# Kernel tuning notes

Measured on AMD Instinct MI355X. Metric: run time of the kernel, lower is better.

Reference implementation:

```python
import jax, jax.numpy as jnp
import numpy as np

N = 96        # num_nodes
D = 64        # emb_size / n_hid
BS = 16
T = 13
G = 1         # num_graph

# all N^2 ordered pairs, receiver-major: edge e=i*N+j has receiver i, sender j
_REC = jnp.repeat(jnp.arange(N), N)
_SEND = jnp.tile(jnp.arange(N), N)


def _lin(shape, key, scale=0.05):
    return (jax.random.normal(key, shape, dtype=jnp.float32) * scale)


def setup_inputs() -> dict:
    key = jax.random.key(0)
    ks = jax.random.split(key, 24)
    inp = {
        "skill_seq": jax.random.randint(ks[0], (BS, T), 0, N, dtype=jnp.int32),
        "adj": jax.random.uniform(ks[1], (G, BS, N, N), dtype=jnp.float32),
        "node_embeddings": jax.random.normal(ks[2], (G, N, D), dtype=jnp.float32),
        # edge MLP
        "W_msg1": _lin((2 * D, D), ks[3]), "b_msg1": jnp.zeros((D,), jnp.float32),
        "W_msg2": _lin((D, D), ks[4]),     "b_msg2": jnp.zeros((D,), jnp.float32),
        # GRU hidden projections (no bias)
        "W_hr": _lin((D, D), ks[5]), "W_hi": _lin((D, D), ks[6]), "W_hh": _lin((D, D), ks[7]),
        # GRU input projections (bias)
        "W_ir": _lin((D, D), ks[8]),  "b_ir": jnp.zeros((D,), jnp.float32),
        "W_ii": _lin((D, D), ks[9]),  "b_ii": jnp.zeros((D,), jnp.float32),
        "W_in": _lin((D, D), ks[10]), "b_in": jnp.zeros((D,), jnp.float32),
        # output MLP
        "W_o1": _lin((D, D), ks[11]), "b_o1": jnp.zeros((D,), jnp.float32),
        "W_o2": _lin((D, D), ks[12]), "b_o2": jnp.zeros((D,), jnp.float32),
        "W_o3": _lin((D, D), ks[13]), "b_o3": jnp.zeros((D,), jnp.float32),
    }
    return inp


def _forward(skill_seq, adj, node_embeddings,
             W_msg1, b_msg1, W_msg2, b_msg2,
             W_hr, W_hi, W_hh,
             W_ir, b_ir, W_ii, b_ii, W_in, b_in,
             W_o1, b_o1, W_o2, b_o2, W_o3, b_o3):
    bs, time_steps = skill_seq.shape
    hidden0 = jnp.zeros((G, bs, N, D), dtype=adj.dtype)
    emb = node_embeddings[0]  # [N, D] (num_graph=1)

    def step(hidden, skill_t):
        # gather senders/receivers over the node axis -> [G, bs, N^2, 2D]
        senders = hidden[:, :, _SEND, :]
        receivers = hidden[:, :, _REC, :]
        pre_msg = jnp.concatenate([senders, receivers], axis=-1)
        msg = jnp.tanh(pre_msg @ W_msg1 + b_msg1)        # [G, bs, N^2, D]
        msg = jnp.tanh(msg @ W_msg2 + b_msg2)
        msg = msg.reshape(G, bs, N, N, D)                # receiver i, sender j
        # mask by adjacency and scatter-sum over senders, then /N
        agg = jnp.einsum('gbij,gbijd->gbid', adj, msg) / N   # [G, bs, N, D]
        inputs = emb[skill_t][None, :, None, :]          # [1, bs, 1, D]
        r = jax.nn.sigmoid(inputs @ W_ir + b_ir + agg @ W_hr)
        i = jax.nn.sigmoid(inputs @ W_ii + b_ii + agg @ W_hi)
        n = jnp.tanh(inputs @ W_in + b_in + r * (agg @ W_hh))
        hidden = (1.0 - i) * n + i * hidden
        pred = jax.nn.relu(hidden @ W_o1 + b_o1)
        pred = jax.nn.relu(pred @ W_o2 + b_o2)
        pred = pred @ W_o3 + b_o3                        # [G, bs, N, D]
        return hidden, pred

    skills_t = skill_seq[:, :time_steps - 1].T           # [T-1, bs]
    _, preds = jax.lax.scan(step, hidden0, skills_t)     # [T-1, G, bs, N, D]
    # torch: stack(dim=1) -> [G, T-1, bs, N, D]; transpose(1,2) -> [G, bs, T-1, N, D]
    return jnp.transpose(preds, (1, 2, 0, 3, 4))


def reference(skill_seq, adj, node_embeddings,
              W_msg1, b_msg1, W_msg2, b_msg2,
              W_hr, W_hi, W_hh,
              W_ir, b_ir, W_ii, b_ii, W_in, b_in,
              W_o1, b_o1, W_o2, b_o2, W_o3, b_o3):
    return _forward(skill_seq, adj, node_embeddings,
                    W_msg1, b_msg1, W_msg2, b_msg2,
                    W_hr, W_hi, W_hh,
                    W_ir, b_ir, W_ii, b_ii, W_in, b_in,
                    W_o1, b_o1, W_o2, b_o2, W_o3, b_o3)
```

## Files before the change

### kernel.cpp

```cpp
#include <hip/hip_runtime.h>

typedef unsigned short ushort_t;
typedef __attribute__((ext_vector_type(8))) short short8;
typedef __attribute__((ext_vector_type(4))) float floatx4;

#define NN 96
#define DD 64
#define BSZ 16
#define TSTEP 12
#define JSPLIT 8
#define JPW 12
#define ITILES 6

#define OFF_HID   0u
#define OFF_S     393216u
#define OFF_R     786432u
#define OFF_E     1179648u
#define OFF_PART  1253376u
#define OFF_WSWZ  4399104u

static __device__ __forceinline__ short f2bf(float f){
    union { float f; unsigned u; } v; v.f = f;
    unsigned u = v.u;
    u += 0x7fffu + ((u >> 16) & 1u);
    return (short)(u >> 16);
}
static __device__ __forceinline__ float fast_tanh(float x){
    x = fminf(20.f, fmaxf(-20.f, x));
    float p = __expf(2.f * x);
    return (p - 1.f) * __builtin_amdgcn_rcpf(p + 1.f);
}
static __device__ __forceinline__ float fast_sigmoid(float x){
    x = fminf(30.f, fmaxf(-30.f, x));
    float p = __expf(-x);
    return __builtin_amdgcn_rcpf(1.f + p);
}
static __device__ __forceinline__ void zero4(floatx4* a){
    floatx4 z = {0.f,0.f,0.f,0.f};
    a[0]=z; a[1]=z; a[2]=z; a[3]=z;
}
static __device__ __forceinline__ void buildA(const float* sM, int col, int quad, short8& a0, short8& a1){
    floatx4 f0 = *(const floatx4*)&sM[col*68 + quad*8];
    floatx4 f1 = *(const floatx4*)&sM[col*68 + quad*8 + 4];
    floatx4 f2 = *(const floatx4*)&sM[col*68 + 32 + quad*8];
    floatx4 f3 = *(const floatx4*)&sM[col*68 + 32 + quad*8 + 4];
    #pragma unroll
    for (int jj = 0; jj < 4; jj++){
        a0[jj]   = f2bf(f0[jj]);
        a0[4+jj] = f2bf(f1[jj]);
        a1[jj]   = f2bf(f2[jj]);
        a1[4+jj] = f2bf(f3[jj]);
    }
}
static __device__ __forceinline__ void mm16(short8 a0, short8 a1, const short8* wzm, int l, floatx4* acc){
    #pragma unroll
    for (int nt = 0; nt < 4; nt++){
        short8 b0 = wzm[nt*64 + l];
        short8 b1 = wzm[(4 + nt)*64 + l];
        acc[nt] = __builtin_amdgcn_mfma_f32_16x16x32_bf16(a0, b0, acc[nt], 0, 0, 0);
        acc[nt] = __builtin_amdgcn_mfma_f32_16x16x32_bf16(a1, b1, acc[nt], 0, 0, 0);
    }
}

__global__ __launch_bounds__(256) void k_init(
    const float* __restrict__ emb, const float* __restrict__ Wmsg1,
    const float* __restrict__ Wmsg2,
    const float* __restrict__ Whr, const float* __restrict__ Whi, const float* __restrict__ Whh,
    const float* __restrict__ Wir, const float* __restrict__ bir,
    const float* __restrict__ Wii, const float* __restrict__ bii,
    const float* __restrict__ Win, const float* __restrict__ bin,
    const float* __restrict__ Wo1, const float* __restrict__ Wo2, const float* __restrict__ Wo3,
    float* __restrict__ wsf, float* __restrict__ Ef, ushort_t* __restrict__ wswz)
{
    int wg = blockIdx.x, tid = threadIdx.x;
    if (wg < 288) {
        floatx4 z = {0.f,0.f,0.f,0.f};
        ((floatx4*)wsf)[wg*256 + tid] = z;
    } else if (wg < 360) {
        int flat = (wg - 288)*256 + tid;
        int m = flat / 6144; int r = flat % 6144; int s = r >> 6; int d = r & 63;
        const float* W = (m==0)? Wir : (m==1)? Wii : Win;
        const float* B = (m==0)? bir : (m==1)? bii : bin;
        float acc = B[d];
        #pragma unroll 8
        for (int k = 0; k < 64; k++)
            acc += emb[s*64 + k] * W[k*64 + d];
        Ef[flat] = acc;
    } else {
        int flat = (wg - 360)*256 + tid;
        int m = flat >> 12; int q = flat & 4095;
        int jj = q & 7, lane = (q >> 3) & 63, nt = (q >> 9) & 3, kc = q >> 11;
        int k = kc*32 + ((lane >> 4) << 3) + jj;
        int n = nt*16 + (lane & 15);
        const float* src; int idx = k*64 + n;
        switch (m) {
          case 0: src = Wmsg2; break;
          case 1: src = Whr;  break;
          case 2: src = Whi;  break;
          case 3: src = Whh;  break;
          case 4: src = Wmsg1; break;
          case 5: src = Wmsg1; idx = (64 + k)*64 + n; break;
          case 6: src = Wo1; break;
          case 7: src = Wo2; break;
          default: src = Wo3; break;
        }
        wswz[flat] = (ushort_t)f2bf(src[idx]);
    }
}

__global__ __launch_bounds__(256) void k_msg(
    const float* __restrict__ adj, const float* __restrict__ b1in, const float* __restrict__ b2in,
    const float* __restrict__ Sg, const float* __restrict__ Rg,
    const ushort_t* __restrict__ wswz, float* __restrict__ partial)
{
    __shared__ float sS[JPW*64];
    __shared__ float sRB[16*68];
    __shared__ float sAdj[16*JPW];
    __shared__ float sAgg[4][16*68];
    int wg = blockIdx.x;
    int js = wg / 96; int rem = wg % 96; int b = rem / 6; int it = rem % 6;
    int tid = threadIdx.x; int w = tid >> 6; int l = tid & 63;
    int quad = l >> 4, col = l & 15;
    int j0 = js * JPW;

    for (int q = tid; q < JPW*16; q += 256) {
        int row = q >> 4, c4 = (q & 15) * 4;
        *(floatx4*)&sS[row*64 + c4] = *(const floatx4*)&Sg[(b*NN + j0 + row)*64 + c4];
    }
    for (int q = tid; q < 16*16; q += 256) {
        int row = q >> 4, c4 = (q & 15) * 4;
        floatx4 r4 = *(const floatx4*)&Rg[(b*NN + it*16 + row)*64 + c4];
        floatx4 b4 = *(const floatx4*)&b1in[c4];
        floatx4 o = r4 + b4;
        *(floatx4*)&sRB[row*68 + c4] = o;
    }
    for (int q = tid; q < 16*JPW; q += 256) {
        int i = q / JPW, j = q % JPW;
        sAdj[q] = adj[(b*NN + it*16 + i)*NN + j0 + j];
    }
    const short8* wz = (const short8*)wswz;
    short8 w2f[2][4];
    #pragma unroll
    for (int kc = 0; kc < 2; kc++)
      #pragma unroll
      for (int nt = 0; nt < 4; nt++)
        w2f[kc][nt] = wz[(kc*4 + nt)*64 + l];
    float b2v[4];
    #pragma unroll
    for (int nt = 0; nt < 4; nt++) b2v[nt] = b2in[nt*16 + col];
    __syncthreads();

    float rbv[16];
    #pragma unroll
    for (int c = 0; c < 4; c++)
        *(floatx4*)&rbv[c*4] = *(const floatx4*)&sRB[col*68 + (c>>1)*32 + quad*8 + (c&1)*4];

    float agg[4][4];
    #pragma unroll
    for (int nt=0;nt<4;nt++)
      #pragma unroll
      for (int r=0;r<4;r++) agg[nt][r] = 0.f;

    for (int c = 0; c < 3; c++) {
        int jl = w*3 + c;
        float sv[16];
        #pragma unroll
        for (int cc = 0; cc < 4; cc++)
            *(floatx4*)&sv[cc*4] = *(const floatx4*)&sS[jl*64 + (cc>>1)*32 + quad*8 + (cc&1)*4];
        short8 a0, a1;
        #pragma unroll
        for (int e = 0; e < 8; e++) {
            a0[e] = f2bf(fast_tanh(sv[e]   + rbv[e]));
            a1[e] = f2bf(fast_tanh(sv[8+e] + rbv[8+e]));
        }
        floatx4 acc[4];
        zero4(acc);
        #pragma unroll
        for (int nt = 0; nt < 4; nt++) {
            acc[nt] = __builtin_amdgcn_mfma_f32_16x16x32_bf16(a0, w2f[0][nt], acc[nt], 0,0,0);
            acc[nt] = __builtin_amdgcn_mfma_f32_16x16x32_bf16(a1, w2f[1][nt], acc[nt], 0,0,0);
        }
        float adjv[4];
        #pragma unroll
        for (int r = 0; r < 4; r++) adjv[r] = sAdj[(quad*4 + r)*JPW + jl];
        #pragma unroll
        for (int nt = 0; nt < 4; nt++)
          #pragma unroll
          for (int r = 0; r < 4; r++)
            agg[nt][r] += adjv[r] * fast_tanh(acc[nt][r] + b2v[nt]);
    }
    #pragma unroll
    for (int nt = 0; nt < 4; nt++)
      #pragma unroll
      for (int r = 0; r < 4; r++)
        sAgg[w][(quad*4 + r)*68 + nt*16 + col] = agg[nt][r];
    __syncthreads();
    {
        int i = tid >> 4, k4 = (tid & 15) * 4;
        floatx4 s0 = *(const floatx4*)&sAgg[0][i*68 + k4];
        floatx4 s1 = *(const floatx4*)&sAgg[1][i*68 + k4];
        floatx4 s2 = *(const floatx4*)&sAgg[2][i*68 + k4];
        floatx4 s3 = *(const floatx4*)&sAgg[3][i*68 + k4];
        floatx4 o = (s0 + s1) + (s2 + s3);
        o = o * (1.f/96.f);
        *(floatx4*)&partial[((js*BSZ + b)*NN + it*16 + i)*64 + k4] = o;
    }
}

__global__ __launch_bounds__(64) void k_gru(
    const int* __restrict__ skills, const float* __restrict__ partial,
    const float* __restrict__ Ef, const ushort_t* __restrict__ wswz,
    const float* __restrict__ bo1, const float* __restrict__ bo2, const float* __restrict__ bo3,
    float* __restrict__ hidden, float* __restrict__ Sg, float* __restrict__ Rg,
    float* __restrict__ out, int t)
{
    __shared__ float sM[16*68];
    int wg = blockIdx.x; int b = wg / 6, it = wg % 6;
    int l = threadIdx.x; int quad = l >> 4, col = l & 15;
    {
        int i = l >> 2, k4 = (l & 3) * 16;
        floatx4 a[4];
        zero4(a);
        for (int p = 0; p < JSPLIT; p++) {
            const float* base = &partial[((p*BSZ + b)*NN + it*16 + i)*64 + k4];
            #pragma unroll
            for (int cc = 0; cc < 4; cc++)
                a[cc] += *(const floatx4*)&base[cc*4];
        }
        #pragma unroll
        for (int cc = 0; cc < 4; cc++)
            *(floatx4*)&sM[i*68 + k4 + cc*4] = a[cc];
    }
    __syncthreads();
    short8 aggA0, aggA1;
    buildA(sM, col, quad, aggA0, aggA1);

    floatx4 Ar[4], Ai[4], Ah[4];
    zero4(Ar); zero4(Ai); zero4(Ah);
    mm16(aggA0, aggA1, (const short8*)wswz + 1*512, l, Ar);
    mm16(aggA0, aggA1, (const short8*)wswz + 2*512, l, Ai);
    mm16(aggA0, aggA1, (const short8*)wswz + 3*512, l, Ah);

    int s = skills[b*13 + t];
    const float* Er = Ef + 0*6144 + s*64;
    const float* Ei = Ef + 1*6144 + s*64;
    const float* En = Ef + 2*6144 + s*64;

    float hnew[4][4];
    #pragma unroll
    for (int nt = 0; nt < 4; nt++) {
      #pragma unroll
      for (int r = 0; r < 4; r++) {
        int d = nt*16 + col;
        int row = it*16 + quad*4 + r;
        float gr = fast_sigmoid(Er[d] + Ar[nt][r]);
        float gi = fast_sigmoid(Ei[d] + Ai[nt][r]);
        float nn = fast_tanh(En[d] + gr * Ah[nt][r]);
        float hold = hidden[(b*NN + row)*64 + d];
        float h = (1.f - gi)*nn + gi*hold;
        hidden[(b*NN + row)*64 + d] = h;
        hnew[nt][r] = h;
      }
    }
    __syncthreads();
    #pragma unroll
    for (int nt = 0; nt < 4; nt++)
      #pragma unroll
      for (int r = 0; r < 4; r++)
        sM[(quad*4 + r)*68 + nt*16 + col] = hnew[nt][r];
    __syncthreads();
    short8 hA0, hA1;
    buildA(sM, col, quad, hA0, hA1);

    floatx4 Sa[4], Ra[4];
    zero4(Sa); zero4(Ra);
    mm16(hA0, hA1, (const short8*)wswz + 4*512, l, Sa);
    mm16(hA0, hA1, (const short8*)wswz + 5*512, l, Ra);
    #pragma unroll
    for (int nt = 0; nt < 4; nt++)
      #pragma unroll
      for (int r = 0; r < 4; r++) {
        int d = nt*16 + col;
        int row = it*16 + quad*4 + r;
        Sg[(b*NN + row)*64 + d] = Sa[nt][r];
        Rg[(b*NN + row)*64 + d] = Ra[nt][r];
      }

    floatx4 O1[4]; zero4(O1);
    mm16(hA0, hA1, (const short8*)wswz + 6*512, l, O1);
    __syncthreads();
    #pragma unroll
    for (int nt = 0; nt < 4; nt++)
      #pragma unroll
      for (int r = 0; r < 4; r++)
        sM[(quad*4 + r)*68 + nt*16 + col] = fmaxf(0.f, O1[nt][r] + bo1[nt*16 + col]);
    __syncthreads();
    short8 p1A0, p1A1; buildA(sM, col, quad, p1A0, p1A1);
    floatx4 O2[4]; zero4(O2);
    mm16(p1A0, p1A1, (const short8*)wswz + 7*512, l, O2);
    __syncthreads();
    #pragma unroll
    for (int nt = 0; nt < 4; nt++)
      #pragma unroll
      for (int r = 0; r < 4; r++)
        sM[(quad*4 + r)*68 + nt*16 + col] = fmaxf(0.f, O2[nt][r] + bo2[nt*16 + col]);
    __syncthreads();
    short8 p2A0, p2A1; buildA(sM, col, quad, p2A0, p2A1);
    floatx4 O3[4]; zero4(O3);
    mm16(p2A0, p2A1, (const short8*)wswz + 8*512, l, O3);
    #pragma unroll
    for (int nt = 0; nt < 4; nt++)
      #pragma unroll
      for (int r = 0; r < 4; r++) {
        int d = nt*16 + col;
        int row = quad*4 + r;
        float v = O3[nt][r] + bo3[d];
        out[((b*TSTEP + t)*NN + it*16 + row)*64 + d] = v;
      }
}

extern "C" void kernel_launch(void* const* d_in, const int* in_sizes, int n_in,
                              void* d_out, int out_size, void* d_ws, size_t ws_size,
                              hipStream_t stream) {
    const int*   skills = (const int*)d_in[0];
    const float* adj    = (const float*)d_in[1];
    const float* emb    = (const float*)d_in[2];
    const float* Wmsg1  = (const float*)d_in[3];
    const float* b1     = (const float*)d_in[4];
    const float* Wmsg2  = (const float*)d_in[5];
    const float* b2     = (const float*)d_in[6];
    const float* Whr    = (const float*)d_in[7];
    const float* Whi    = (const float*)d_in[8];
    const float* Whh    = (const float*)d_in[9];
    const float* Wir    = (const float*)d_in[10];
    const float* bir    = (const float*)d_in[11];
    const float* Wii    = (const float*)d_in[12];
    const float* bii    = (const float*)d_in[13];
    const float* Win    = (const float*)d_in[14];
    const float* bin    = (const float*)d_in[15];
    const float* Wo1    = (const float*)d_in[16];
    const float* bo1    = (const float*)d_in[17];
    const float* Wo2    = (const float*)d_in[18];
    const float* bo2    = (const float*)d_in[19];
    const float* Wo3    = (const float*)d_in[20];
    const float* bo3    = (const float*)d_in[21];

    char* ws = (char*)d_ws;
    float*    hidden  = (float*)(ws + OFF_HID);
    float*    Sg      = (float*)(ws + OFF_S);
    float*    Rg      = (float*)(ws + OFF_R);
    float*    Ef      = (float*)(ws + OFF_E);
    float*    partial = (float*)(ws + OFF_PART);
    ushort_t* wswz    = (ushort_t*)(ws + OFF_WSWZ);
    float*    out     = (float*)d_out;

    k_init<<<dim3(504), dim3(256), 0, stream>>>(emb, Wmsg1, Wmsg2, Whr, Whi, Whh,
        Wir, bir, Wii, bii, Win, bin, Wo1, Wo2, Wo3, (float*)ws, Ef, wswz);

    for (int t = 0; t < TSTEP; t++) {
        k_msg<<<dim3(JSPLIT*BSZ*ITILES), dim3(256), 0, stream>>>(adj, b1, b2, Sg, Rg, wswz, partial);
        k_gru<<<dim3(BSZ*ITILES), dim3(64), 0, stream>>>(skills, partial, Ef, wswz,
            bo1, bo2, bo3, hidden, Sg, Rg, out, t);
    }
}
```

Before: 294.5 us.

## Split output MLP out of recurrent GRU step and batch it after loop

The GRU step kernel no longer computes the three-layer output MLP. Instead it stores every timestep's hidden state in a history buffer, and a single k_out kernel runs the MLP over all timesteps at the end. The GRU kernel now uses 256 threads, with separate waves computing the three gate matmuls and the S/R projections in parallel, and weight fragments are preloaded into registers. This shortens the serial critical path of each recurrent step, at the cost of a larger workspace and one extra launch.

```diff
diff --git a/kernel.cpp b/kernel.cpp
--- a/kernel.cpp
+++ b/kernel.cpp
@@ -12,12 +12,13 @@
 #define JPW 12
 #define ITILES 6
 
-#define OFF_HID   0u
-#define OFF_S     393216u
-#define OFF_R     786432u
-#define OFF_E     1179648u
-#define OFF_PART  1253376u
-#define OFF_WSWZ  4399104u
+#define OFF_HALL  0u
+#define OFF_S     5111808u
+#define OFF_R     5505024u
+#define OFF_E     5898240u
+#define OFF_PART  5971968u
+#define OFF_WSWZ  9117696u
+#define HSLOT     98304
 
 static __device__ __forceinline__ short f2bf(float f){
     union { float f; unsigned u; } v; v.f = f;
@@ -59,6 +60,13 @@
         short8 b1 = wzm[(4 + nt)*64 + l];
         acc[nt] = __builtin_amdgcn_mfma_f32_16x16x32_bf16(a0, b0, acc[nt], 0, 0, 0);
         acc[nt] = __builtin_amdgcn_mfma_f32_16x16x32_bf16(a1, b1, acc[nt], 0, 0, 0);
+    }
+}
+static __device__ __forceinline__ void mm16r(short8 a0, short8 a1, const short8* f, floatx4* acc){
+    #pragma unroll
+    for (int nt = 0; nt < 4; nt++){
+        acc[nt] = __builtin_amdgcn_mfma_f32_16x16x32_bf16(a0, f[nt],     acc[nt], 0, 0, 0);
+        acc[nt] = __builtin_amdgcn_mfma_f32_16x16x32_bf16(a1, f[4 + nt], acc[nt], 0, 0, 0);
     }
 }
 
@@ -70,12 +78,15 @@
     const float* __restrict__ Wii, const float* __restrict__ bii,
     const float* __restrict__ Win, const float* __restrict__ bin,
     const float* __restrict__ Wo1, const float* __restrict__ Wo2, const float* __restrict__ Wo3,
-    float* __restrict__ wsf, float* __restrict__ Ef, ushort_t* __restrict__ wswz)
+    float* __restrict__ hz, float* __restrict__ SRz,
+    float* __restrict__ Ef, ushort_t* __restrict__ wswz)
 {
     int wg = blockIdx.x, tid = threadIdx.x;
     if (wg < 288) {
+        int flat = wg*256 + tid;
         floatx4 z = {0.f,0.f,0.f,0.f};
-        ((floatx4*)wsf)[wg*256 + tid] = z;
+        if (flat < 24576) ((floatx4*)hz)[flat] = z;
+        else              ((floatx4*)SRz)[flat - 24576] = z;
     } else if (wg < 360) {
         int flat = (wg - 288)*256 + tid;
         int m = flat / 6144; int r = flat % 6144; int s = r >> 6; int d = r & 63;
@@ -207,116 +218,146 @@
     }
 }
 
-__global__ __launch_bounds__(64) void k_gru(
+__global__ __launch_bounds__(256) void k_gru(
     const int* __restrict__ skills, const float* __restrict__ partial,
     const float* __restrict__ Ef, const ushort_t* __restrict__ wswz,
-    const float* __restrict__ bo1, const float* __restrict__ bo2, const float* __restrict__ bo3,
-    float* __restrict__ hidden, float* __restrict__ Sg, float* __restrict__ Rg,
-    float* __restrict__ out, int t)
+    const float* __restrict__ hprev, float* __restrict__ hcur,
+    float* __restrict__ Sg, float* __restrict__ Rg, int t)
 {
     __shared__ float sM[16*68];
+    __shared__ float sG[3][16*68];
+    __shared__ float sH[16*64];
+    __shared__ float sE[3][64];
     int wg = blockIdx.x; int b = wg / 6, it = wg % 6;
-    int l = threadIdx.x; int quad = l >> 4, col = l & 15;
+    int tid = threadIdx.x; int w = tid >> 6; int l = tid & 63;
+    int quad = l >> 4, col = l & 15;
+    int i = tid >> 4, k4 = (tid & 15) * 4;
+
+    const short8* wzb = (const short8*)wswz;
+    short8 fG[8], fSR[8];
+    if (w < 3) {
+        #pragma unroll
+        for (int q = 0; q < 8; q++) fG[q] = wzb[(1 + w)*512 + q*64 + l];
+    }
+    if (w < 2) {
+        #pragma unroll
+        for (int q = 0; q < 8; q++) fSR[q] = wzb[(4 + w)*512 + q*64 + l];
+    }
+
     {
-        int i = l >> 2, k4 = (l & 3) * 16;
-        floatx4 a[4];
-        zero4(a);
-        for (int p = 0; p < JSPLIT; p++) {
-            const float* base = &partial[((p*BSZ + b)*NN + it*16 + i)*64 + k4];
-            #pragma unroll
-            for (int cc = 0; cc < 4; cc++)
-                a[cc] += *(const floatx4*)&base[cc*4];
+        floatx4 a = {0.f,0.f,0.f,0.f};
+        #pragma unroll
+        for (int p = 0; p < JSPLIT; p++)
+            a += *(const floatx4*)&partial[((p*BSZ + b)*NN + it*16 + i)*64 + k4];
+        *(floatx4*)&sM[i*68 + k4] = a;
+        *(floatx4*)&sH[i*64 + k4] = *(const floatx4*)&hprev[(b*NN + it*16 + i)*64 + k4];
+    }
+    if (tid < 192) {
+        int s = skills[b*13 + t];
+        ((float*)sE)[tid] = Ef[(tid >> 6)*6144 + s*64 + (tid & 63)];
+    }
+    __syncthreads();
+
+    if (w < 3) {
+        short8 a0, a1;
+        buildA(sM, col, quad, a0, a1);
+        floatx4 acc[4];
+        zero4(acc);
+        mm16r(a0, a1, fG, acc);
+        #pragma unroll
+        for (int nt = 0; nt < 4; nt++)
+          #pragma unroll
+          for (int r = 0; r < 4; r++)
+            sG[w][(quad*4 + r)*68 + nt*16 + col] = acc[nt][r];
+    }
+    __syncthreads();
+
+    {
+        float h[4];
+        #pragma unroll
+        for (int e = 0; e < 4; e++) {
+            int d = k4 + e;
+            float gr = fast_sigmoid(sE[0][d] + sG[0][i*68 + d]);
+            float gi = fast_sigmoid(sE[1][d] + sG[1][i*68 + d]);
+            float nv = fast_tanh(sE[2][d] + gr * sG[2][i*68 + d]);
+            h[e] = (1.f - gi)*nv + gi*sH[i*64 + d];
         }
         #pragma unroll
+        for (int e = 0; e < 4; e++) sM[i*68 + k4 + e] = h[e];
+        floatx4 hv = { h[0], h[1], h[2], h[3] };
+        *(floatx4*)&hcur[(b*NN + it*16 + i)*64 + k4] = hv;
+    }
+    __syncthreads();
+
+    if (w < 2) {
+        short8 a0, a1;
+        buildA(sM, col, quad, a0, a1);
+        floatx4 acc[4];
+        zero4(acc);
+        mm16r(a0, a1, fSR, acc);
+        float* dst = (w == 0) ? Sg : Rg;
+        #pragma unroll
+        for (int nt = 0; nt < 4; nt++)
+          #pragma unroll
+          for (int r = 0; r < 4; r++)
+            dst[(b*NN + it*16 + quad*4 + r)*64 + nt*16 + col] = acc[nt][r];
+    }
+}
+
+__global__ __launch_bounds__(256) void k_out(
+    const float* __restrict__ hall, const ushort_t* __restrict__ wswz,
+    const float* __restrict__ bo1, const float* __restrict__ bo2, const float* __restrict__ bo3,
+    float* __restrict__ out)
+{
+    __shared__ float sT[4][16*68];
+    int tid = threadIdx.x; int w = tid >> 6; int l = tid & 63;
+    int quad = l >> 4, col = l & 15;
+    int g = blockIdx.x*4 + w;
+    int ts = g / 96; int rem = g % 96; int b = rem / 6, it = rem % 6;
+    const float* hsrc = hall + (size_t)(ts + 1)*HSLOT + (b*NN + it*16)*64;
+    float* sm = sT[w];
+    {
+        int i = l >> 2, c0 = (l & 3) * 16;
+        #pragma unroll
         for (int cc = 0; cc < 4; cc++)
-            *(floatx4*)&sM[i*68 + k4 + cc*4] = a[cc];
-    }
-    __syncthreads();
-    short8 aggA0, aggA1;
-    buildA(sM, col, quad, aggA0, aggA1);
-
-    floatx4 Ar[4], Ai[4], Ah[4];
-    zero4(Ar); zero4(Ai); zero4(Ah);
-    mm16(aggA0, aggA1, (const short8*)wswz + 1*512, l, Ar);
-    mm16(aggA0, aggA1, (const short8*)wswz + 2*512, l, Ai);
-    mm16(aggA0, aggA1, (const short8*)wswz + 3*512, l, Ah);
-
-    int s = skills[b*13 + t];
-    const float* Er = Ef + 0*6144 + s*64;
-    const float* Ei = Ef + 1*6144 + s*64;
-    const float* En = Ef + 2*6144 + s*64;
-
-    float hnew[4][4];
+            *(floatx4*)&sm[i*68 + c0 + cc*4] = *(const floatx4*)&hsrc[i*64 + c0 + cc*4];
+    }
+    float bv1[4], bv2[4], bv3[4];
     #pragma unroll
     for (int nt = 0; nt < 4; nt++) {
-      #pragma unroll
-      for (int r = 0; r < 4; r++) {
-        int d = nt*16 + col;
-        int row = it*16 + quad*4 + r;
-        float gr = fast_sigmoid(Er[d] + Ar[nt][r]);
-        float gi = fast_sigmoid(Ei[d] + Ai[nt][r]);
-        float nn = fast_tanh(En[d] + gr * Ah[nt][r]);
-        float hold = hidden[(b*NN + row)*64 + d];
-        float h = (1.f - gi)*nn + gi*hold;
-        hidden[(b*NN + row)*64 + d] = h;
-        hnew[nt][r] = h;
-      }
-    }
-    __syncthreads();
+        bv1[nt] = bo1[nt*16 + col];
+        bv2[nt] = bo2[nt*16 + col];
+        bv3[nt] = bo3[nt*16 + col];
+    }
+    short8 a0, a1;
+    floatx4 acc[4];
+
+    buildA(sm, col, quad, a0, a1);
+    zero4(acc);
+    mm16(a0, a1, (const short8*)wswz + 6*512, l, acc);
     #pragma unroll
     for (int nt = 0; nt < 4; nt++)
       #pragma unroll
       for (int r = 0; r < 4; r++)
-        sM[(quad*4 + r)*68 + nt*16 + col] = hnew[nt][r];
-    __syncthreads();
-    short8 hA0, hA1;
-    buildA(sM, col, quad, hA0, hA1);
-
-    floatx4 Sa[4], Ra[4];
-    zero4(Sa); zero4(Ra);
-    mm16(hA0, hA1, (const short8*)wswz + 4*512, l, Sa);
-    mm16(hA0, hA1, (const short8*)wswz + 5*512, l, Ra);
+        sm[(quad*4 + r)*68 + nt*16 + col] = fmaxf(0.f, acc[nt][r] + bv1[nt]);
+
+    buildA(sm, col, quad, a0, a1);
+    zero4(acc);
+    mm16(a0, a1, (const short8*)wswz + 7*512, l, acc);
     #pragma unroll
     for (int nt = 0; nt < 4; nt++)
       #pragma unroll
-      for (int r = 0; r < 4; r++) {
-        int d = nt*16 + col;
-        int row = it*16 + quad*4 + r;
-        Sg[(b*NN + row)*64 + d] = Sa[nt][r];
-        Rg[(b*NN + row)*64 + d] = Ra[nt][r];
-      }
-
-    floatx4 O1[4]; zero4(O1);
-    mm16(hA0, hA1, (const short8*)wswz + 6*512, l, O1);
-    __syncthreads();
+      for (int r = 0; r < 4; r++)
+        sm[(quad*4 + r)*68 + nt*16 + col] = fmaxf(0.f, acc[nt][r] + bv2[nt]);
+
+    buildA(sm, col, quad, a0, a1);
+    zero4(acc);
+    mm16(a0, a1, (const short8*)wswz + 8*512, l, acc);
     #pragma unroll
     for (int nt = 0; nt < 4; nt++)
       #pragma unroll
       for (int r = 0; r < 4; r++)
-        sM[(quad*4 + r)*68 + nt*16 + col] = fmaxf(0.f, O1[nt][r] + bo1[nt*16 + col]);
-    __syncthreads();
-    short8 p1A0, p1A1; buildA(sM, col, quad, p1A0, p1A1);
-    floatx4 O2[4]; zero4(O2);
-    mm16(p1A0, p1A1, (const short8*)wswz + 7*512, l, O2);
-    __syncthreads();
-    #pragma unroll
-    for (int nt = 0; nt < 4; nt++)
-      #pragma unroll
-      for (int r = 0; r < 4; r++)
-        sM[(quad*4 + r)*68 + nt*16 + col] = fmaxf(0.f, O2[nt][r] + bo2[nt*16 + col]);
-    __syncthreads();
-    short8 p2A0, p2A1; buildA(sM, col, quad, p2A0, p2A1);
-    floatx4 O3[4]; zero4(O3);
-    mm16(p2A0, p2A1, (const short8*)wswz + 8*512, l, O3);
-    #pragma unroll
-    for (int nt = 0; nt < 4; nt++)
-      #pragma unroll
-      for (int r = 0; r < 4; r++) {
-        int d = nt*16 + col;
-        int row = quad*4 + r;
-        float v = O3[nt][r] + bo3[d];
-        out[((b*TSTEP + t)*NN + it*16 + row)*64 + d] = v;
-      }
+        out[((b*TSTEP + ts)*NN + it*16 + quad*4 + r)*64 + nt*16 + col] = acc[nt][r] + bv3[nt];
 }
 
 extern "C" void kernel_launch(void* const* d_in, const int* in_sizes, int n_in,
@@ -346,7 +387,7 @@
     const float* bo3    = (const float*)d_in[21];
 
     char* ws = (char*)d_ws;
-    float*    hidden  = (float*)(ws + OFF_HID);
+    float*    hall    = (float*)(ws + OFF_HALL);
     float*    Sg      = (float*)(ws + OFF_S);
     float*    Rg      = (float*)(ws + OFF_R);
     float*    Ef      = (float*)(ws + OFF_E);
@@ -355,11 +396,12 @@
     float*    out     = (float*)d_out;
 
     k_init<<<dim3(504), dim3(256), 0, stream>>>(emb, Wmsg1, Wmsg2, Whr, Whi, Whh,
-        Wir, bir, Wii, bii, Win, bin, Wo1, Wo2, Wo3, (float*)ws, Ef, wswz);
+        Wir, bir, Wii, bii, Win, bin, Wo1, Wo2, Wo3, hall, Sg, Ef, wswz);
 
     for (int t = 0; t < TSTEP; t++) {
         k_msg<<<dim3(JSPLIT*BSZ*ITILES), dim3(256), 0, stream>>>(adj, b1, b2, Sg, Rg, wswz, partial);
-        k_gru<<<dim3(BSZ*ITILES), dim3(64), 0, stream>>>(skills, partial, Ef, wswz,
-            bo1, bo2, bo3, hidden, Sg, Rg, out, t);
-    }
-}
+        k_gru<<<dim3(BSZ*ITILES), dim3(256), 0, stream>>>(skills, partial, Ef, wswz,
+            hall + (size_t)t*HSLOT, hall + (size_t)(t+1)*HSLOT, Sg, Rg, t);
+    }
+    k_out<<<dim3(288), dim3(256), 0, stream>>>(hall, wswz, bo1, bo2, bo3, out);
+}
```

Measured after the change: 273.5 us. 1.08x faster.
